# Kernel tuning notes

Hardware: AMD Instinct MI355X
Metric: run time of the kernel (lower is better)

The kernel has to match this reference:

```python
import jax, jax.numpy as jnp
import numpy as np

RADIUS = 0.15
NSAMPLE = 128
NPOINT = 128
EPS = 1e-5  # BatchNorm eps (eval mode, running_mean=0, running_var=1)


def _bn(x, g, b):
    shape = (1, -1) + (1,) * (x.ndim - 2)
    return x * (g / jnp.sqrt(1.0 + EPS)).reshape(shape) + b.reshape(shape)


def _fps(x, npoint):
    # farthest point sampling; x: (Bk, N, 3) -> (Bk, npoint) int32
    Bn, N, _ = x.shape

    def step(carry, _):
        dist, far = carry
        c = jnp.take_along_axis(x, far[:, None, None], 1)  # (Bk,1,3)
        d = jnp.sum((x - c) ** 2, -1)
        dist = jnp.minimum(dist, d)
        return (dist, jnp.argmax(dist, -1).astype(jnp.int32)), far

    init = (jnp.full((Bn, N), 1e10, x.dtype), jnp.zeros((Bn,), jnp.int32))
    _, idxs = jax.lax.scan(step, init, None, length=npoint)
    return idxs.T  # (Bk, npoint)


def _sa_module(x, f, mlp):
    # PointnetSAModuleVotes: FPS -> ball query -> group (use_xyz, normalize_xyz)
    # -> shared MLP (conv2d 1x1 + BN + ReLU) -> max over nsample.
    Bk, M, _ = x.shape
    fps_idx = _fps(x, NPOINT)
    new_xyz = jnp.take_along_axis(x, fps_idx[..., None], 1)  # (Bk,np,3)
    d2 = jnp.sum((new_xyz[:, :, None, :] - x[:, None, :, :]) ** 2, -1)  # (Bk,np,M)
    cand = jnp.where(d2 < RADIUS ** 2, jnp.arange(M)[None, None, :], M)
    cand = jnp.sort(cand, -1)[..., :NSAMPLE]  # first nsample in-radius indices
    first = cand[..., :1]
    first = jnp.where(first == M, 0, first)
    idx = jnp.where(cand == M, first, cand)  # (Bk,np,ns), pad with first valid
    gx = jnp.take_along_axis(x, idx.reshape(Bk, -1)[..., None], 1).reshape(Bk, NPOINT, NSAMPLE, 3)
    gxn = (gx - new_xyz[:, :, None, :]) / RADIUS  # normalize_xyz=True
    gf = jnp.take_along_axis(f[:, :, None, :], idx[:, None, :, :], 3)  # (Bk,C,np,ns)
    h = jnp.concatenate([gxn.transpose(0, 3, 1, 2), gf], 1)  # (Bk, C+3, np, ns)
    for (w, b, g, be) in mlp:
        h = jax.nn.relu(_bn(jnp.einsum('oc,bcps->bops', w, h) + b[None, :, None, None], g, be))
    return new_xyz, h.max(-1)  # (Bk,np,3), (Bk,128,np)


def setup_inputs() -> dict:
    key = jax.random.key(0)
    ks = iter(jax.random.split(key, 40))
    B, M, K, C = 2, 1024, 19, 256
    inp = {}
    inp['xyz'] = jax.random.normal(next(ks), (B, M, K, 3), jnp.float32)
    inp['features'] = jax.random.normal(next(ks), (B, C, K, M), jnp.float32)

    def conv_p(prefix, cin, cout):
        inp[prefix + '_w'] = jax.random.normal(next(ks), (cout, cin), jnp.float32) * (1.0 / np.sqrt(cin))
        inp[prefix + '_b'] = jax.random.normal(next(ks), (cout,), jnp.float32) * 0.02
        inp[prefix + '_g'] = 1.0 + 0.1 * jax.random.normal(next(ks), (cout,), jnp.float32)
        inp[prefix + '_be'] = 0.02 * jax.random.normal(next(ks), (cout,), jnp.float32)

    conv_p('m1', C + 3, 128)  # use_xyz -> 259 in-channels
    conv_p('m2', 128, 128)
    conv_p('m3', 128, 128)
    conv_p('c1', 128, 128)
    conv_p('c2', 128, 128)
    inp['op_w'] = jax.random.normal(next(ks), (K, 5, 128), jnp.float32) * (1.0 / np.sqrt(128))
    inp['op_b'] = jax.random.normal(next(ks), (K, 5), jnp.float32) * 0.02
    return inp


def reference(xyz, features, m1_w, m1_b, m1_g, m1_be, m2_w, m2_b, m2_g, m2_be,
              m3_w, m3_b, m3_g, m3_be, c1_w, c1_b, c1_g, c1_be,
              c2_w, c2_b, c2_g, c2_be, op_w, op_b):
    B, M, K, _ = xyz.shape
    C = features.shape[1]
    # fold vote_factor k into the batch dim (all per-k SA/conv weights are shared)
    x = xyz.transpose(0, 2, 1, 3).reshape(B * K, M, 3)
    f = features.transpose(0, 2, 1, 3).reshape(B * K, C, M)
    mlp = [(m1_w, m1_b, m1_g, m1_be), (m2_w, m2_b, m2_g, m2_be), (m3_w, m3_b, m3_g, m3_be)]
    new_xyz, feat = _sa_module(x, f, mlp)
    net = jax.nn.relu(_bn(jnp.einsum('oc,bcp->bop', c1_w, feat) + c1_b[None, :, None], c1_g, c1_be))
    net = jax.nn.relu(_bn(jnp.einsum('oc,bcp->bop', c2_w, net) + c2_b[None, :, None], c2_g, c2_be))
    net = net.reshape(B, K, 128, NPOINT)
    # per-k output conv (conv_op ModuleList), 128 -> 2+3
    out = jnp.einsum('koc,bkcp->bkop', op_w, net) + op_b[None, :, :, None]
    net_t = out.transpose(0, 1, 3, 2)  # (B,K,np,5)
    agg_xyz = new_xyz.reshape(B, K, NPOINT, 3)
    center = agg_xyz + net_t[..., 2:5]  # decode_scores_
    scores = jnp.concatenate([net_t[..., :2], center], -1)  # obj(2) + center(3)
    return scores, agg_xyz, feat.reshape(B, K, 128, NPOINT)
```

## Files before the change

### kernel.cpp

```cpp
#include <hip/hip_runtime.h>
#include <math.h>

#define NBK   38

#define OFF_XC    0u
#define OFF_NXYZ  466944u
#define OFF_BIDX  525312u
#define OFF_W1F   3015680u
#define OFF_PREP  22938624u
#define OFF_WF    22955008u
#define OFF_CNT   23348224u

#define OUT_AGG   24320
#define OUT_FEAT  38912

typedef short bf16x8 __attribute__((ext_vector_type(8)));
typedef float f32x4  __attribute__((ext_vector_type(4)));
typedef int   v4i    __attribute__((ext_vector_type(4)));
typedef int   v2i    __attribute__((ext_vector_type(2)));

__device__ __forceinline__ float dist2f(float a0, float a1, float a2,
                                        float b0, float b1, float b2) {
#pragma clang fp contract(off)
  float d0 = a0 - b0;
  float d1 = a1 - b1;
  float d2 = a2 - b2;
  return d0 * d0 + d1 * d1 + d2 * d2;
}

__device__ __forceinline__ void split2rn(float v, unsigned& sh, unsigned& sm) {
  unsigned u = __float_as_uint(v);
  unsigned rh = (u + 0x7fffu + ((u >> 16) & 1u)) & 0xffff0000u;
  sh = rh >> 16;
  float r1 = v - __uint_as_float(rh);
  unsigned u1 = __float_as_uint(r1);
  unsigned rm = (u1 + 0x7fffu + ((u1 >> 16) & 1u)) & 0xffff0000u;
  sm = rm >> 16;
}

#define DPP_FMAX_STEP(v, ctrl)                                                 \
  {                                                                            \
    int _s = __builtin_amdgcn_update_dpp(__float_as_int(v), __float_as_int(v), \
                                         (ctrl), 0xf, 0xf, false);             \
    (v) = fmaxf((v), __int_as_float(_s));                                      \
  }

__device__ __forceinline__ float readlane_f(float v, int l) {
  return __int_as_float(__builtin_amdgcn_readlane(__float_as_int(v), l));
}

__global__ __launch_bounds__(512, 2) void front_kernel(
    const float* __restrict__ xyz, const float* __restrict__ feats,
    const float* __restrict__ m1w, const float* __restrict__ m1b,
    const float* __restrict__ m1g, const float* __restrict__ m1be,
    const float* __restrict__ m2w, const float* __restrict__ m2b,
    const float* __restrict__ m2g, const float* __restrict__ m2be,
    const float* __restrict__ m3w, const float* __restrict__ m3b,
    const float* __restrict__ m3g, const float* __restrict__ m3be,
    const float* __restrict__ c1w, const float* __restrict__ c1b,
    const float* __restrict__ c1g, const float* __restrict__ c1be,
    const float* __restrict__ c2w, const float* __restrict__ c2b,
    const float* __restrict__ c2g, const float* __restrict__ c2be,
    float* __restrict__ xc, float* __restrict__ nxyz, float* __restrict__ agg,
    int* __restrict__ bidx, int* __restrict__ counts,
    float* __restrict__ W1f, short* __restrict__ Wf, float* __restrict__ prep)
{
  __shared__ __align__(16) char smem[32768];
  int bid = blockIdx.x, t = threadIdx.x;
  int wave = t >> 6, lane = t & 63;

  if (bid < NBK) {
    int bk = bid;
    int b = bk / 19, k = bk % 19;
    float4* sp4 = (float4*)smem;
    float4* scen4 = (float4*)(smem + 16384);
    int* sfar = (int*)(smem + 18432);
    int2* cexch = (int2*)(smem + 18944);

    for (int i = t; i < 1024; i += 512) {
      const float* src = xyz + ((size_t)((b * 1024 + i) * 19 + k)) * 3;
      float x0 = src[0], x1 = src[1], x2 = src[2];
      sp4[i] = make_float4(x0, x1, x2, 0.f);
      xc[(bk * 3 + 0) * 1024 + i] = x0;
      xc[(bk * 3 + 1) * 1024 + i] = x1;
      xc[(bk * 3 + 2) * 1024 + i] = x2;
    }
    if (t == 0) sfar[0] = 0;
    __syncthreads();

    float px[8], py[8], pz[8], dist[8];
    if (wave < 2) {
      __builtin_amdgcn_s_setprio(1);
      int mbase = (wave << 9) + (lane << 3);
#pragma unroll
      for (int j = 0; j < 8; ++j) {
        float4 p = sp4[mbase + j];
        px[j] = p.x; py[j] = p.y; pz[j] = p.z;
        dist[j] = 1e10f;
      }
    }

    int far = 0;
    for (int it = 1; it < 128; ++it) {
      if (wave < 2) {
        float4 c = sp4[far];
#pragma unroll
        for (int j = 0; j < 8; ++j) {
          float d = dist2f(px[j], py[j], pz[j], c.x, c.y, c.z);
          dist[j] = fminf(dist[j], d);
        }
        float tv[4]; int tj[4];
#pragma unroll
        for (int i = 0; i < 4; ++i) {
          bool L = dist[2 * i] >= dist[2 * i + 1];
          tv[i] = L ? dist[2 * i] : dist[2 * i + 1];
          tj[i] = L ? (2 * i) : (2 * i + 1);
        }
        {
          bool L0 = tv[0] >= tv[1];
          float v0 = L0 ? tv[0] : tv[1]; int j0 = L0 ? tj[0] : tj[1];
          bool L1 = tv[2] >= tv[3];
          float v1 = L1 ? tv[2] : tv[3]; int j1 = L1 ? tj[2] : tj[3];
          bool L = v0 >= v1;
          tv[0] = L ? v0 : v1; tj[0] = L ? j0 : j1;
        }
        float lmax = tv[0];
        float g = lmax;
        DPP_FMAX_STEP(g, 0x111);
        DPP_FMAX_STEP(g, 0x112);
        DPP_FMAX_STEP(g, 0x114);
        DPP_FMAX_STEP(g, 0x118);
        float r0 = readlane_f(g, 15);
        float r1 = readlane_f(g, 31);
        float r2 = readlane_f(g, 47);
        float r3 = readlane_f(g, 63);
        float gmax = fmaxf(fmaxf(r0, r1), fmaxf(r2, r3));
        unsigned long long mk = __ballot(lmax == gmax);
        int wl = (int)__builtin_ctzll(mk);
        int lj = (lane << 3) + tj[0];
        int cand_m = (wave << 9) + __builtin_amdgcn_readlane(lj, wl);
        if (lane == 0) cexch[(it & 1) * 2 + wave] =
            make_int2(__float_as_int(gmax), cand_m);
      }
      __syncthreads();
      if (wave < 2) {
        int2 c0 = cexch[(it & 1) * 2 + 0];
        int2 c1 = cexch[(it & 1) * 2 + 1];
        far = (__int_as_float(c1.x) > __int_as_float(c0.x)) ? c1.y : c0.y;
        if (t == 0) sfar[it] = far;
      }
    }
    if (wave < 2) __builtin_amdgcn_s_setprio(0);
    __syncthreads();

    if (t < 128) {
      float4 c = sp4[sfar[t]];
      scen4[t] = c;
      nxyz[bk * 384 + t * 3 + 0] = c.x;
      nxyz[bk * 384 + t * 3 + 1] = c.y;
      nxyz[bk * 384 + t * 3 + 2] = c.z;
      agg[bk * 384 + t * 3 + 0] = c.x;
      agg[bk * 384 + t * 3 + 1] = c.y;
      agg[bk * 384 + t * 3 + 2] = c.z;
    }
    __syncthreads();

    for (int p = wave * 16; p < wave * 16 + 16; ++p) {
      float4 cen = scen4[p];
      int* outp = bidx + ((size_t)(bk * 128 + p)) * 128;
      int count = 0, first = 0;
      bool got = false;
      for (int ch = 0; ch < 16 && count < 128; ++ch) {
        int m = (ch << 6) + lane;
        float4 pv = sp4[m];
        float d = dist2f(pv.x, pv.y, pv.z, cen.x, cen.y, cen.z);
        bool flag = d < 0.0225f;
        unsigned long long mask = __ballot(flag);
        if (!got && mask) { first = (ch << 6) + __builtin_ctzll(mask); got = true; }
        int pos = count + (int)__popcll(mask & ((1ull << lane) - 1ull));
        if (flag && pos < 128) outp[pos] = m;
        count += (int)__popcll(mask);
      }
      for (int j = count + lane; j < 128; j += 64) outp[j] = first;
      if (lane == 0) counts[bk * 128 + p] = count > 128 ? 128 : count;
    }
    return;
  }

  if (bid < 190) {
    short* ffrag = (short*)smem;
    int blk = bid - NBK;
    int bk = blk >> 2, mq = blk & 3;
    int b = bk / 19, k = bk % 19;
    int quad = lane >> 4, nl = lane & 15;
    int mloc = t & 127, cq = t >> 7;
    int chalf = cq >> 1, ghalf = cq & 1;
    int st_w = mloc >> 4, sl_w = mloc & 15;

    for (int half = 0; half < 2; ++half) {
      int m0 = (mq << 8) + (half << 7);
      const float* fbase = feats + ((size_t)(b * 4864 + k)) * 1024 + m0 + mloc;

      f32x4 acc[8];
#pragma unroll
      for (int st = 0; st < 8; ++st) acc[st] = (f32x4){0.f, 0.f, 0.f, 0.f};

      for (int ch = 0; ch < 4; ++ch) {
        int cbase = ch * 64 + chalf * 32;
#pragma unroll
        for (int g2 = 0; g2 < 2; ++g2) {
          int g = ghalf * 2 + g2;
          float v[8];
#pragma unroll
          for (int j = 0; j < 8; ++j)
            v[j] = fbase[(size_t)(cbase + g * 8 + j) * 19456];
          unsigned sh[8], sm[8];
#pragma unroll
          for (int j = 0; j < 8; ++j) split2rn(v[j], sh[j], sm[j]);
          int base = chalf * 4096 + st_w * 512 + (g * 16 + sl_w) * 8;
          v4i ph = {(int)(sh[0] | (sh[1] << 16)), (int)(sh[2] | (sh[3] << 16)),
                    (int)(sh[4] | (sh[5] << 16)), (int)(sh[6] | (sh[7] << 16))};
          *(v4i*)&ffrag[base] = ph;
          v4i pm = {(int)(sm[0] | (sm[1] << 16)), (int)(sm[2] | (sm[3] << 16)),
                    (int)(sm[4] | (sm[5] << 16)), (int)(sm[6] | (sm[7] << 16))};
          *(v4i*)&ffrag[base + 8192] = pm;
        }
        __syncthreads();
#pragma unroll
        for (int kkl = 0; kkl < 2; ++kkl) {
          int kk = ch * 2 + kkl;
          bf16x8 a0, a1;
          {
            int o_row = wave * 16 + nl;
            const float* wsrc = m1w + o_row * 259 + 3 + kk * 32 + quad * 8;
            float wv[8];
#pragma unroll
            for (int j = 0; j < 8; ++j) wv[j] = wsrc[j];
            unsigned sh[8], sm[8];
#pragma unroll
            for (int j = 0; j < 8; ++j) split2rn(wv[j], sh[j], sm[j]);
            short ah[8], am[8];
#pragma unroll
            for (int j = 0; j < 8; ++j) { ah[j] = (short)sh[j]; am[j] = (short)sm[j]; }
            a0 = (bf16x8){ah[0], ah[1], ah[2], ah[3], ah[4], ah[5], ah[6], ah[7]};
            a1 = (bf16x8){am[0], am[1], am[2], am[3], am[4], am[5], am[6], am[7]};
          }
#pragma unroll
          for (int st = 0; st < 8; ++st) {
            const short* hb = ffrag + kkl * 4096 + st * 512 + lane * 8;
            bf16x8 b0 = *(const bf16x8*)hb;
            bf16x8 b1 = *(const bf16x8*)(hb + 8192);
            f32x4 c = acc[st];
            c = __builtin_amdgcn_mfma_f32_16x16x32_bf16(a1, b0, c, 0, 0, 0);
            c = __builtin_amdgcn_mfma_f32_16x16x32_bf16(a0, b1, c, 0, 0, 0);
            c = __builtin_amdgcn_mfma_f32_16x16x32_bf16(a0, b0, c, 0, 0, 0);
            acc[st] = c;
          }
        }
        __syncthreads();
      }
      float inv = 1.0f / sqrtf(1.0f + 1e-5f);
      int o0 = wave * 16 + quad * 4;
      float4 bb = *(const float4*)&m1b[o0];
      float4 gg = *(const float4*)&m1g[o0];
#pragma unroll
      for (int st = 0; st < 8; ++st) {
        int m_out = m0 + st * 16 + nl;
        f32x4 cc = acc[st];
        float4 r;
        r.x = (cc[0] + bb.x) * (gg.x * inv);
        r.y = (cc[1] + bb.y) * (gg.y * inv);
        r.z = (cc[2] + bb.z) * (gg.z * inv);
        r.w = (cc[3] + bb.w) * (gg.w * inv);
        *(float4*)&W1f[((size_t)(bk * 1024 + m_out)) * 128 + o0] = r;
      }
    }
    return;
  }

  if (bid < 206) {
    int idx = (bid - 190) * 512 + t;
#pragma unroll
    for (int e = 0; e < 4; ++e) {
      int i = idx * 4 + e;
      int c = i & 127, o = (i >> 7) & 127, l = i >> 14;
      float w = (l ? m3w : m2w)[o * 128 + c];
      unsigned sh, sm;
      split2rn(w, sh, sm);
      int ot = o >> 4, mm = o & 15, kk = c >> 5, q = (c & 31) >> 3, j = c & 7;
      int within = (q * 16 + mm) * 8 + j;
      Wf[(((l * 2 + 0) * 4 + kk) * 8 + ot) * 512 + within] = (short)sh;
      Wf[(((l * 2 + 1) * 4 + kk) * 8 + ot) * 512 + within] = (short)sm;
    }
    return;
  }

  if (bid < 222) {
    int idx2 = (bid - 206) * 512 + t;
#pragma unroll
    for (int e = 0; e < 4; ++e) {
      int i = idx2 * 4 + e;
      int c = i & 127, o = (i >> 7) & 127, l = i >> 14;
      float w = (l ? c2w : c1w)[o * 128 + c];
      unsigned sh, sm;
      split2rn(w, sh, sm);
      int ot = o >> 4, mm = o & 15, kk = c >> 5, q = (c & 31) >> 3, j = c & 7;
      int within = (q * 16 + mm) * 8 + j;
      Wf[131072 + (((l * 2 + 0) * 4 + kk) * 8 + ot) * 512 + within] = (short)sh;
      Wf[131072 + (((l * 2 + 1) * 4 + kk) * 8 + ot) * 512 + within] = (short)sm;
    }
    return;
  }

  if (t < 128) {
    float inv = 1.0f / sqrtf(1.0f + 1e-5f);
    float a1 = m1g[t] * inv;
    prep[t] = a1;
    float a2 = m2g[t] * inv;  prep[256 + t] = a2;  prep[384 + t] = fmaf(m2b[t], a2, m2be[t]);
    float a3 = m3g[t] * inv;  prep[512 + t] = a3;  prep[640 + t] = fmaf(m3b[t], a3, m3be[t]);
    float ac1 = c1g[t] * inv; prep[768 + t] = ac1; prep[896 + t] = fmaf(c1b[t], ac1, c1be[t]);
    float ac2 = c2g[t] * inv; prep[1024 + t] = ac2; prep[1152 + t] = fmaf(c2b[t], ac2, c2be[t]);
    prep[1280 + 4 * t + 0] = m1w[t * 259 + 0] * a1;
    prep[1280 + 4 * t + 1] = m1w[t * 259 + 1] * a1;
    prep[1280 + 4 * t + 2] = m1w[t * 259 + 2] * a1;
    prep[1280 + 4 * t + 3] = m1be[t];
  }
}

__device__ __forceinline__ void mfma_layer(const short* __restrict__ Wf,
                                           const short* hfrag, int l,
                                           int wave, int lane, int nst_h,
                                           f32x4 acc[2][4])
{
#pragma unroll 1
  for (int kk = 0; kk < 4; ++kk) {
    bf16x8 a[2][2];
#pragma unroll
    for (int oi = 0; oi < 2; ++oi)
#pragma unroll
      for (int sp = 0; sp < 2; ++sp)
        a[oi][sp] = *(const bf16x8*)(Wf + (((l * 2 + sp) * 4 + kk) * 8 + (wave * 2 + oi)) * 512 + lane * 8);
    for (int st = 0; st < nst_h; ++st) {
      const short* hb = hfrag + kk * 2048 + st * 512 + lane * 8;
      bf16x8 b0 = *(const bf16x8*)(hb);
      bf16x8 b1 = *(const bf16x8*)(hb + 8192);
#pragma unroll
      for (int oi = 0; oi < 2; ++oi) {
        f32x4 c = acc[oi][st];
        c = __builtin_amdgcn_mfma_f32_16x16x32_bf16(a[oi][1], b0, c, 0, 0, 0);
        c = __builtin_amdgcn_mfma_f32_16x16x32_bf16(a[oi][0], b1, c, 0, 0, 0);
        c = __builtin_amdgcn_mfma_f32_16x16x32_bf16(a[oi][0], b0, c, 0, 0, 0);
        acc[oi][st] = c;
      }
    }
  }
}

__global__ __launch_bounds__(256, 3) void sa_kernel(
    const float* __restrict__ xc, const float* __restrict__ nxyz,
    const int* __restrict__ bidx, const int* __restrict__ counts,
    const float* __restrict__ W1f, const float* __restrict__ prep,
    const short* __restrict__ Wf, float* __restrict__ feat_out)
{
  __shared__ __align__(16) short hfrag[16384];
  __shared__ float pcs[512];
  __shared__ float sm[32 * 128];
  __shared__ float ccen[12];
  __shared__ int scnt[4];
  int gb = blockIdx.x, bk = gb >> 5, pb = (gb & 31) << 2;
  int t = threadIdx.x;
  int wave = t >> 6, lane = t & 63;
  int quad = lane >> 4, nl = lane & 15;

  pcs[t] = prep[1280 + t];
  pcs[256 + t] = prep[1536 + t];
  if (t < 4) scnt[t] = counts[bk * 128 + pb + t];
  if (t < 12) {
    int bb = t / 3, c = t % 3;
    ccen[t] = nxyz[(bk * 128 + pb + bb) * 3 + c];
  }
  __syncthreads();
  int n0 = (scnt[0] + 15) >> 4, n1 = (scnt[1] + 15) >> 4;
  int n2 = (scnt[2] + 15) >> 4, n3 = (scnt[3] + 15) >> 4;
  int pf1 = n0, pf2 = n0 + n1, pf3 = n0 + n1 + n2, T = n0 + n1 + n2 + n3;

  for (int q0 = 0; q0 < T; q0 += 4) {
    int nst_h = T - q0;
    if (nst_h > 4) nst_h = 4;
    {
      int cg = wave;
      int st = lane >> 4, sl = lane & 15;
      if (st < nst_h) {
        int q = q0 + st;
        int bq = (q >= pf1) + (q >= pf2) + (q >= pf3);
        int tstart = (bq == 0) ? 0 : (bq == 1) ? pf1 : (bq == 2) ? pf2 : pf3;
        int tslot = q - tstart;
        int m = bidx[((size_t)(bk * 128 + pb + bq)) * 128 + tslot * 16 + sl];
        float cen0 = ccen[bq * 3 + 0], cen1 = ccen[bq * 3 + 1], cen2 = ccen[bq * 3 + 2];
        float g0 = (xc[(bk * 3 + 0) * 1024 + m] - cen0) * (1.0f / 0.15f);
        float g1 = (xc[(bk * 3 + 1) * 1024 + m] - cen1) * (1.0f / 0.15f);
        float g2 = (xc[(bk * 3 + 2) * 1024 + m] - cen2) * (1.0f / 0.15f);
        const float4* wrow = (const float4*)(W1f + ((size_t)(bk * 1024 + m)) * 128 + cg * 32);
        const float4* pcp = (const float4*)pcs + cg * 32;
#pragma unroll
        for (int g = 0; g < 4; ++g) {
          float4 wva = wrow[g * 2], wvb = wrow[g * 2 + 1];
          float wv[8] = {wva.x, wva.y, wva.z, wva.w, wvb.x, wvb.y, wvb.z, wvb.w};
          unsigned sh[8], smv[8];
#pragma unroll
          for (int e = 0; e < 8; ++e) {
            float4 pc = pcp[g * 8 + e];
            float hv = fmaxf(wv[e] + pc.x * g0 + pc.y * g1 + pc.z * g2 + pc.w, 0.f);
            split2rn(hv, sh[e], smv[e]);
          }
          int base = (cg * 4 + st) * 512 + (g * 16 + sl) * 8;
          v4i ph = {(int)(sh[0] | (sh[1] << 16)), (int)(sh[2] | (sh[3] << 16)),
                    (int)(sh[4] | (sh[5] << 16)), (int)(sh[6] | (sh[7] << 16))};
          *(v4i*)&hfrag[base] = ph;
          v4i pm = {(int)(smv[0] | (smv[1] << 16)), (int)(smv[2] | (smv[3] << 16)),
                    (int)(smv[4] | (smv[5] << 16)), (int)(smv[6] | (smv[7] << 16))};
          *(v4i*)&hfrag[base + 8192] = pm;
        }
      }
    }
    __syncthreads();

    f32x4 acc[2][4];
#pragma unroll
    for (int oi = 0; oi < 2; ++oi)
#pragma unroll
      for (int st = 0; st < 4; ++st) acc[oi][st] = (f32x4){0.f, 0.f, 0.f, 0.f};
    mfma_layer(Wf, hfrag, 0, wave, lane, nst_h, acc);
    __syncthreads();

#pragma unroll
    for (int oi = 0; oi < 2; ++oi) {
      int o0 = (wave * 2 + oi) * 16 + quad * 4;
      float4 al = *(const float4*)&prep[256 + o0];
      float4 be = *(const float4*)&prep[384 + o0];
      int kk2 = o0 >> 5, g2 = (o0 & 31) >> 3, j0 = o0 & 7;
      for (int st = 0; st < nst_h; ++st) {
        f32x4 cc = acc[oi][st];
        float v0 = fmaxf(fmaf(cc[0], al.x, be.x), 0.f);
        float v1 = fmaxf(fmaf(cc[1], al.y, be.y), 0.f);
        float v2 = fmaxf(fmaf(cc[2], al.z, be.z), 0.f);
        float v3 = fmaxf(fmaf(cc[3], al.w, be.w), 0.f);
        unsigned h0, m0_, h1, m1_, h2, m2_, h3, m3_;
        split2rn(v0, h0, m0_); split2rn(v1, h1, m1_);
        split2rn(v2, h2, m2_); split2rn(v3, h3, m3_);
        int base = (kk2 * 4 + st) * 512 + (g2 * 16 + nl) * 8 + j0;
        v2i w0 = {(int)(h0 | (h1 << 16)), (int)(h2 | (h3 << 16))};
        *(v2i*)&hfrag[base] = w0;
        v2i w1 = {(int)(m0_ | (m1_ << 16)), (int)(m2_ | (m3_ << 16))};
        *(v2i*)&hfrag[base + 8192] = w1;
      }
    }
    __syncthreads();

#pragma unroll
    for (int oi = 0; oi < 2; ++oi)
#pragma unroll
      for (int st = 0; st < 4; ++st) acc[oi][st] = (f32x4){0.f, 0.f, 0.f, 0.f};
    mfma_layer(Wf, hfrag, 1, wave, lane, nst_h, acc);

#pragma unroll
    for (int oi = 0; oi < 2; ++oi) {
      int o0 = (wave * 2 + oi) * 16 + quad * 4;
      float4 al = *(const float4*)&prep[512 + o0];
      float4 be = *(const float4*)&prep[640 + o0];
      for (int st = 0; st < nst_h; ++st) {
        f32x4 cc = acc[oi][st];
        float v[4];
        v[0] = fmaxf(fmaf(cc[0], al.x, be.x), 0.f);
        v[1] = fmaxf(fmaf(cc[1], al.y, be.y), 0.f);
        v[2] = fmaxf(fmaf(cc[2], al.z, be.z), 0.f);
        v[3] = fmaxf(fmaf(cc[3], al.w, be.w), 0.f);
#pragma unroll
        for (int r = 0; r < 4; ++r) {
          float x = v[r];
          x = fmaxf(x, __shfl_xor(x, 1));
          x = fmaxf(x, __shfl_xor(x, 2));
          x = fmaxf(x, __shfl_xor(x, 4));
          x = fmaxf(x, __shfl_xor(x, 8));
          if (nl == 0) sm[(q0 + st) * 128 + o0 + r] = x;
        }
      }
    }
    __syncthreads();
  }

#pragma unroll
  for (int e = t; e < 512; e += 256) {
    int bb = e >> 7, o = e & 127;
    int qs = (bb == 0) ? 0 : (bb == 1) ? pf1 : (bb == 2) ? pf2 : pf3;
    int nq = (bb == 0) ? n0 : (bb == 1) ? n1 : (bb == 2) ? n2 : n3;
    float v = sm[qs * 128 + o];
    for (int q = 1; q < nq; ++q) v = fmaxf(v, sm[(qs + q) * 128 + o]);
    feat_out[(((size_t)bk) << 14) + (o << 7) + pb + bb] = v;
  }
}

__global__ __launch_bounds__(256) void head_kernel(const float* __restrict__ featg,
    const float* __restrict__ prep, const short* __restrict__ Wf,
    const float* __restrict__ nxyz, const float* __restrict__ opw,
    const float* __restrict__ opb, float* __restrict__ scores)
{
  __shared__ __align__(16) short hfrag[16384];
  __shared__ float hplain[128 * 65];
  int bk = blockIdx.x >> 1, p0 = (blockIdx.x & 1) << 6;
  int t = threadIdx.x;
  int wave = t >> 6, lane = t & 63;
  int quad = lane >> 4, nl = lane & 15;
  const short* WC = Wf + 131072;

  {
    int cg = wave;
    int st = lane >> 4, sl = lane & 15;
    const float* fb = featg + (bk << 14) + p0 + lane;
#pragma unroll
    for (int g = 0; g < 4; ++g) {
      float v[8];
#pragma unroll
      for (int e = 0; e < 8; ++e)
        v[e] = fb[(cg * 32 + g * 8 + e) << 7];
      unsigned sh[8], sm[8];
#pragma unroll
      for (int e = 0; e < 8; ++e) split2rn(v[e], sh[e], sm[e]);
      int base = (cg * 4 + st) * 512 + (g * 16 + sl) * 8;
      v4i ph = {(int)(sh[0] | (sh[1] << 16)), (int)(sh[2] | (sh[3] << 16)),
                (int)(sh[4] | (sh[5] << 16)), (int)(sh[6] | (sh[7] << 16))};
      *(v4i*)&hfrag[base] = ph;
      v4i pm = {(int)(sm[0] | (sm[1] << 16)), (int)(sm[2] | (sm[3] << 16)),
                (int)(sm[4] | (sm[5] << 16)), (int)(sm[6] | (sm[7] << 16))};
      *(v4i*)&hfrag[base + 8192] = pm;
    }
  }
  __syncthreads();

  f32x4 acc[2][4];
#pragma unroll
  for (int oi = 0; oi < 2; ++oi)
#pragma unroll
    for (int st = 0; st < 4; ++st) acc[oi][st] = (f32x4){0.f, 0.f, 0.f, 0.f};
  mfma_layer(WC, hfrag, 0, wave, lane, 4, acc);
  __syncthreads();

#pragma unroll
  for (int oi = 0; oi < 2; ++oi) {
    int o0 = (wave * 2 + oi) * 16 + quad * 4;
    float4 al = *(const float4*)&prep[768 + o0];
    float4 be = *(const float4*)&prep[896 + o0];
    int kk2 = o0 >> 5, g2 = (o0 & 31) >> 3, j0 = o0 & 7;
#pragma unroll
    for (int st = 0; st < 4; ++st) {
      f32x4 cc = acc[oi][st];
      float v0 = fmaxf(fmaf(cc[0], al.x, be.x), 0.f);
      float v1 = fmaxf(fmaf(cc[1], al.y, be.y), 0.f);
      float v2 = fmaxf(fmaf(cc[2], al.z, be.z), 0.f);
      float v3 = fmaxf(fmaf(cc[3], al.w, be.w), 0.f);
      unsigned h0, m0_, h1, m1_, h2, m2_, h3, m3_;
      split2rn(v0, h0, m0_); split2rn(v1, h1, m1_);
      split2rn(v2, h2, m2_); split2rn(v3, h3, m3_);
      int base = (kk2 * 4 + st) * 512 + (g2 * 16 + nl) * 8 + j0;
      v2i w0 = {(int)(h0 | (h1 << 16)), (int)(h2 | (h3 << 16))};
      *(v2i*)&hfrag[base] = w0;
      v2i w1 = {(int)(m0_ | (m1_ << 16)), (int)(m2_ | (m3_ << 16))};
      *(v2i*)&hfrag[base + 8192] = w1;
    }
  }
  __syncthreads();

#pragma unroll
  for (int oi = 0; oi < 2; ++oi)
#pragma unroll
    for (int st = 0; st < 4; ++st) acc[oi][st] = (f32x4){0.f, 0.f, 0.f, 0.f};
  mfma_layer(WC, hfrag, 1, wave, lane, 4, acc);

#pragma unroll
  for (int oi = 0; oi < 2; ++oi) {
    int o0 = (wave * 2 + oi) * 16 + quad * 4;
    float4 al = *(const float4*)&prep[1024 + o0];
    float4 be = *(const float4*)&prep[1152 + o0];
#pragma unroll
    for (int st = 0; st < 4; ++st) {
      f32x4 cc = acc[oi][st];
      int p = st * 16 + nl;
      hplain[(o0 + 0) * 65 + p] = fmaxf(fmaf(cc[0], al.x, be.x), 0.f);
      hplain[(o0 + 1) * 65 + p] = fmaxf(fmaf(cc[1], al.y, be.y), 0.f);
      hplain[(o0 + 2) * 65 + p] = fmaxf(fmaf(cc[2], al.z, be.z), 0.f);
      hplain[(o0 + 3) * 65 + p] = fmaxf(fmaf(cc[3], al.w, be.w), 0.f);
    }
  }
  __syncthreads();

  if (t < 64) {
    int p = t, k = bk % 19;
    float res[5];
#pragma unroll
    for (int j = 0; j < 5; ++j) {
      const float* wr = opw + ((size_t)(k * 5 + j)) * 128;
      float a = opb[k * 5 + j];
      for (int c = 0; c < 128; ++c) a = fmaf(wr[c], hplain[c * 65 + p], a);
      res[j] = a;
    }
    int pg = p0 + p;
    float a0 = nxyz[(bk * 128 + pg) * 3 + 0];
    float a1 = nxyz[(bk * 128 + pg) * 3 + 1];
    float a2 = nxyz[(bk * 128 + pg) * 3 + 2];
    float* sc = scores + ((size_t)(bk * 128 + pg)) * 5;
    sc[0] = res[0];
    sc[1] = res[1];
    sc[2] = a0 + res[2];
    sc[3] = a1 + res[3];
    sc[4] = a2 + res[4];
  }
}

extern "C" void kernel_launch(void* const* d_in, const int* in_sizes, int n_in,
                              void* d_out, int out_size, void* d_ws, size_t ws_size,
                              hipStream_t stream) {
  (void)in_sizes; (void)n_in; (void)out_size; (void)ws_size;
  const float* xyz  = (const float*)d_in[0];
  const float* fts  = (const float*)d_in[1];
  const float* m1w  = (const float*)d_in[2];
  const float* m1b  = (const float*)d_in[3];
  const float* m1g  = (const float*)d_in[4];
  const float* m1be = (const float*)d_in[5];
  const float* m2w  = (const float*)d_in[6];
  const float* m2b  = (const float*)d_in[7];
  const float* m2g  = (const float*)d_in[8];
  const float* m2be = (const float*)d_in[9];
  const float* m3w  = (const float*)d_in[10];
  const float* m3b  = (const float*)d_in[11];
  const float* m3g  = (const float*)d_in[12];
  const float* m3be = (const float*)d_in[13];
  const float* c1w  = (const float*)d_in[14];
  const float* c1b  = (const float*)d_in[15];
  const float* c1g  = (const float*)d_in[16];
  const float* c1be = (const float*)d_in[17];
  const float* c2w  = (const float*)d_in[18];
  const float* c2b  = (const float*)d_in[19];
  const float* c2g  = (const float*)d_in[20];
  const float* c2be = (const float*)d_in[21];
  const float* opw  = (const float*)d_in[22];
  const float* opb  = (const float*)d_in[23];

  float* out = (float*)d_out;
  char* ws = (char*)d_ws;
  float* xc   = (float*)(ws + OFF_XC);
  float* nxyz = (float*)(ws + OFF_NXYZ);
  int*   bidx = (int*)(ws + OFF_BIDX);
  float* W1f  = (float*)(ws + OFF_W1F);
  float* prep = (float*)(ws + OFF_PREP);
  short* Wf   = (short*)(ws + OFF_WF);
  int*   cnt  = (int*)(ws + OFF_CNT);

  hipLaunchKernelGGL(front_kernel, dim3(223), dim3(512), 0, stream,
                     xyz, fts, m1w, m1b, m1g, m1be, m2w, m2b, m2g, m2be,
                     m3w, m3b, m3g, m3be, c1w, c1b, c1g, c1be,
                     c2w, c2b, c2g, c2be,
                     xc, nxyz, out + OUT_AGG, bidx, cnt, W1f, Wf, prep);
  hipLaunchKernelGGL(sa_kernel, dim3(NBK * 32), dim3(256), 0, stream,
                     xc, nxyz, bidx, cnt, W1f, prep, Wf, out + OUT_FEAT);
  hipLaunchKernelGGL(head_kernel, dim3(NBK * 2), dim3(256), 0, stream,
                     out + OUT_FEAT, prep, Wf, nxyz, opw, opb, out);
}
```

Measured before the change: 283.8 us.

## Spread FPS across all eight waves with two points per lane

Farthest point sampling now uses all 8 waves of the block, each lane holding 2 points instead of 8, in place of only 2 waves each holding 8 points per lane. Each wave publishes its max and index to shared memory, and every thread reduces the 8 candidates after the barrier. This shortens the per-lane serial distance and argmax work on the latency-bound FPS loop, in exchange for a barrier across 8 waves and 8 LDS reads per iteration. The wave priority boost is removed. Tie-breaking still picks the lowest index, since the cross-wave reduction uses a strict greater-than.

```diff
diff --git a/kernel.cpp b/kernel.cpp
--- a/kernel.cpp
+++ b/kernel.cpp
@@ -88,69 +88,55 @@
     if (t == 0) sfar[0] = 0;
     __syncthreads();
 
-    float px[8], py[8], pz[8], dist[8];
-    if (wave < 2) {
-      __builtin_amdgcn_s_setprio(1);
-      int mbase = (wave << 9) + (lane << 3);
-#pragma unroll
-      for (int j = 0; j < 8; ++j) {
-        float4 p = sp4[mbase + j];
-        px[j] = p.x; py[j] = p.y; pz[j] = p.z;
-        dist[j] = 1e10f;
-      }
+    float px[2], py[2], pz[2], dist[2];
+    int mbase = (wave << 7) + (lane << 1);
+#pragma unroll
+    for (int j = 0; j < 2; ++j) {
+      float4 p = sp4[mbase + j];
+      px[j] = p.x; py[j] = p.y; pz[j] = p.z;
+      dist[j] = 1e10f;
     }
 
     int far = 0;
     for (int it = 1; it < 128; ++it) {
-      if (wave < 2) {
-        float4 c = sp4[far];
-#pragma unroll
-        for (int j = 0; j < 8; ++j) {
-          float d = dist2f(px[j], py[j], pz[j], c.x, c.y, c.z);
-          dist[j] = fminf(dist[j], d);
-        }
-        float tv[4]; int tj[4];
-#pragma unroll
-        for (int i = 0; i < 4; ++i) {
-          bool L = dist[2 * i] >= dist[2 * i + 1];
-          tv[i] = L ? dist[2 * i] : dist[2 * i + 1];
-          tj[i] = L ? (2 * i) : (2 * i + 1);
-        }
-        {
-          bool L0 = tv[0] >= tv[1];
-          float v0 = L0 ? tv[0] : tv[1]; int j0 = L0 ? tj[0] : tj[1];
-          bool L1 = tv[2] >= tv[3];
-          float v1 = L1 ? tv[2] : tv[3]; int j1 = L1 ? tj[2] : tj[3];
-          bool L = v0 >= v1;
-          tv[0] = L ? v0 : v1; tj[0] = L ? j0 : j1;
-        }
-        float lmax = tv[0];
-        float g = lmax;
-        DPP_FMAX_STEP(g, 0x111);
-        DPP_FMAX_STEP(g, 0x112);
-        DPP_FMAX_STEP(g, 0x114);
-        DPP_FMAX_STEP(g, 0x118);
-        float r0 = readlane_f(g, 15);
-        float r1 = readlane_f(g, 31);
-        float r2 = readlane_f(g, 47);
-        float r3 = readlane_f(g, 63);
-        float gmax = fmaxf(fmaxf(r0, r1), fmaxf(r2, r3));
-        unsigned long long mk = __ballot(lmax == gmax);
-        int wl = (int)__builtin_ctzll(mk);
-        int lj = (lane << 3) + tj[0];
-        int cand_m = (wave << 9) + __builtin_amdgcn_readlane(lj, wl);
-        if (lane == 0) cexch[(it & 1) * 2 + wave] =
-            make_int2(__float_as_int(gmax), cand_m);
-      }
+      float4 c = sp4[far];
+      float d0 = dist2f(px[0], py[0], pz[0], c.x, c.y, c.z);
+      float d1 = dist2f(px[1], py[1], pz[1], c.x, c.y, c.z);
+      dist[0] = fminf(dist[0], d0);
+      dist[1] = fminf(dist[1], d1);
+      bool L = dist[0] >= dist[1];
+      float lmax = L ? dist[0] : dist[1];
+      int lj = (lane << 1) + (L ? 0 : 1);
+      float g = lmax;
+      DPP_FMAX_STEP(g, 0x111);
+      DPP_FMAX_STEP(g, 0x112);
+      DPP_FMAX_STEP(g, 0x114);
+      DPP_FMAX_STEP(g, 0x118);
+      float r0 = readlane_f(g, 15);
+      float r1 = readlane_f(g, 31);
+      float r2 = readlane_f(g, 47);
+      float r3 = readlane_f(g, 63);
+      float gmax = fmaxf(fmaxf(r0, r1), fmaxf(r2, r3));
+      unsigned long long mk = __ballot(lmax == gmax);
+      int wl = (int)__builtin_ctzll(mk);
+      int cand_m = (wave << 7) + __builtin_amdgcn_readlane(lj, wl);
+      if (lane == 0) cexch[(it & 1) * 8 + wave] =
+          make_int2(__float_as_int(gmax), cand_m);
       __syncthreads();
-      if (wave < 2) {
-        int2 c0 = cexch[(it & 1) * 2 + 0];
-        int2 c1 = cexch[(it & 1) * 2 + 1];
-        far = (__int_as_float(c1.x) > __int_as_float(c0.x)) ? c1.y : c0.y;
-        if (t == 0) sfar[it] = far;
-      }
-    }
-    if (wave < 2) __builtin_amdgcn_s_setprio(0);
+      int2 cc = cexch[(it & 1) * 8 + 0];
+      float bd = __int_as_float(cc.x);
+      int bm = cc.y;
+#pragma unroll
+      for (int w = 1; w < 8; ++w) {
+        int2 cw = cexch[(it & 1) * 8 + w];
+        float dw = __int_as_float(cw.x);
+        bool G = dw > bd;
+        bd = G ? dw : bd;
+        bm = G ? cw.y : bm;
+      }
+      far = bm;
+      if (t == 0) sfar[it] = far;
+    }
     __syncthreads();
 
     if (t < 128) {
```

New measurement: 282.5 us. No clear change (-0.5%).

## Run FPS in a single wave with padded LDS point layout

Applied to the files above, without the earlier changes.

Farthest point sampling now runs in one wavefront holding 16 points per lane instead of two wavefronts. That removes the per-iteration __syncthreads and the shared-memory exchange of candidates between the waves. Points are re-read from LDS every iteration instead of being kept in registers, and the LDS layout is padded by one float4 per 16 entries to avoid bank conflicts on the strided per-lane reads. The cost is twice the serial distance work per lane and extra LDS traffic on the critical FPS loop.

```diff
diff --git a/kernel.cpp b/kernel.cpp
--- a/kernel.cpp
+++ b/kernel.cpp
@@ -72,15 +72,14 @@
   if (bid < NBK) {
     int bk = bid;
     int b = bk / 19, k = bk % 19;
-    float4* sp4 = (float4*)smem;
-    float4* scen4 = (float4*)(smem + 16384);
-    int* sfar = (int*)(smem + 18432);
-    int2* cexch = (int2*)(smem + 18944);
+    float4* sp4p = (float4*)smem;
+    float4* scen4 = (float4*)(smem + 17408);
+    int* sfar = (int*)(smem + 19456);
 
     for (int i = t; i < 1024; i += 512) {
       const float* src = xyz + ((size_t)((b * 1024 + i) * 19 + k)) * 3;
       float x0 = src[0], x1 = src[1], x2 = src[2];
-      sp4[i] = make_float4(x0, x1, x2, 0.f);
+      sp4p[i + (i >> 4)] = make_float4(x0, x1, x2, 0.f);
       xc[(bk * 3 + 0) * 1024 + i] = x0;
       xc[(bk * 3 + 1) * 1024 + i] = x1;
       xc[(bk * 3 + 2) * 1024 + i] = x2;
@@ -88,41 +87,36 @@
     if (t == 0) sfar[0] = 0;
     __syncthreads();
 
-    float px[8], py[8], pz[8], dist[8];
-    if (wave < 2) {
-      __builtin_amdgcn_s_setprio(1);
-      int mbase = (wave << 9) + (lane << 3);
-#pragma unroll
-      for (int j = 0; j < 8; ++j) {
-        float4 p = sp4[mbase + j];
-        px[j] = p.x; py[j] = p.y; pz[j] = p.z;
-        dist[j] = 1e10f;
-      }
-    }
-
-    int far = 0;
-    for (int it = 1; it < 128; ++it) {
-      if (wave < 2) {
-        float4 c = sp4[far];
-#pragma unroll
-        for (int j = 0; j < 8; ++j) {
-          float d = dist2f(px[j], py[j], pz[j], c.x, c.y, c.z);
+    if (wave == 0) {
+      float dist[16];
+#pragma unroll
+      for (int j = 0; j < 16; ++j) dist[j] = 1e10f;
+      int far = 0;
+      for (int it = 1; it < 128; ++it) {
+        float4 c = sp4p[far + (far >> 4)];
+        int bq = lane * 17;
+        asm volatile("" : "+v"(bq));
+#pragma unroll
+        for (int j = 0; j < 16; ++j) {
+          float4 p = sp4p[bq + j];
+          float d = dist2f(p.x, p.y, p.z, c.x, c.y, c.z);
           dist[j] = fminf(dist[j], d);
         }
-        float tv[4]; int tj[4];
-#pragma unroll
-        for (int i = 0; i < 4; ++i) {
+        float tv[8]; int tj[8];
+#pragma unroll
+        for (int i = 0; i < 8; ++i) {
           bool L = dist[2 * i] >= dist[2 * i + 1];
           tv[i] = L ? dist[2 * i] : dist[2 * i + 1];
           tj[i] = L ? (2 * i) : (2 * i + 1);
         }
-        {
-          bool L0 = tv[0] >= tv[1];
-          float v0 = L0 ? tv[0] : tv[1]; int j0 = L0 ? tj[0] : tj[1];
-          bool L1 = tv[2] >= tv[3];
-          float v1 = L1 ? tv[2] : tv[3]; int j1 = L1 ? tj[2] : tj[3];
-          bool L = v0 >= v1;
-          tv[0] = L ? v0 : v1; tj[0] = L ? j0 : j1;
+#pragma unroll
+        for (int s = 1; s < 8; s <<= 1) {
+#pragma unroll
+          for (int i = 0; i < 8; i += 2 * s) {
+            bool L = tv[i] >= tv[i + s];
+            tv[i] = L ? tv[i] : tv[i + s];
+            tj[i] = L ? tj[i] : tj[i + s];
+          }
         }
         float lmax = tv[0];
         float g = lmax;
@@ -137,24 +131,15 @@
         float gmax = fmaxf(fmaxf(r0, r1), fmaxf(r2, r3));
         unsigned long long mk = __ballot(lmax == gmax);
         int wl = (int)__builtin_ctzll(mk);
-        int lj = (lane << 3) + tj[0];
-        int cand_m = (wave << 9) + __builtin_amdgcn_readlane(lj, wl);
-        if (lane == 0) cexch[(it & 1) * 2 + wave] =
-            make_int2(__float_as_int(gmax), cand_m);
-      }
-      __syncthreads();
-      if (wave < 2) {
-        int2 c0 = cexch[(it & 1) * 2 + 0];
-        int2 c1 = cexch[(it & 1) * 2 + 1];
-        far = (__int_as_float(c1.x) > __int_as_float(c0.x)) ? c1.y : c0.y;
-        if (t == 0) sfar[it] = far;
-      }
-    }
-    if (wave < 2) __builtin_amdgcn_s_setprio(0);
+        far = __builtin_amdgcn_readlane((lane << 4) + tj[0], wl);
+        if (lane == 0) sfar[it] = far;
+      }
+    }
     __syncthreads();
 
     if (t < 128) {
-      float4 c = sp4[sfar[t]];
+      int fm = sfar[t];
+      float4 c = sp4p[fm + (fm >> 4)];
       scen4[t] = c;
       nxyz[bk * 384 + t * 3 + 0] = c.x;
       nxyz[bk * 384 + t * 3 + 1] = c.y;
@@ -172,7 +157,7 @@
       bool got = false;
       for (int ch = 0; ch < 16 && count < 128; ++ch) {
         int m = (ch << 6) + lane;
-        float4 pv = sp4[m];
+        float4 pv = sp4p[m + (m >> 4)];
         float d = dist2f(pv.x, pv.y, pv.z, cen.x, cen.y, cen.z);
         bool flag = d < 0.0225f;
         unsigned long long mask = __ballot(flag);
```

Result: slower. 323.5 us (+14.0%).

## Split farthest point sampling into a separate 128-thread kernel before front kernel

Applied to the files above, without the earlier changes.

Moves the FPS loop out of the 512-thread front_kernel blocks into its own kernel with 128-thread blocks, so the per-iteration barrier involves only the two working waves instead of eight mostly idle ones. The front kernel now reloads the point coordinates and sampled centers from global memory for the ball query. This adds a kernel launch and serializes FPS ahead of the other front_kernel work (weight prep etc.), which previously ran concurrently in the other blocks.

```diff
diff --git a/kernel.cpp b/kernel.cpp
--- a/kernel.cpp
+++ b/kernel.cpp
@@ -47,6 +47,95 @@
 
 __device__ __forceinline__ float readlane_f(float v, int l) {
   return __int_as_float(__builtin_amdgcn_readlane(__float_as_int(v), l));
+}
+
+__global__ __launch_bounds__(128, 1) void fps_kernel(
+    const float* __restrict__ xyz, float* __restrict__ xc,
+    float* __restrict__ nxyz, float* __restrict__ agg)
+{
+  __shared__ __align__(16) float4 sp4[1024];
+  __shared__ int2 cexch[2][2];
+  __shared__ int sfar[128];
+  int bk = blockIdx.x;
+  int b = bk / 19, k = bk % 19;
+  int t = threadIdx.x, lane = t & 63, wave = t >> 6;
+
+  for (int i = t; i < 1024; i += 128) {
+    const float* src = xyz + ((size_t)((b * 1024 + i) * 19 + k)) * 3;
+    float x0 = src[0], x1 = src[1], x2 = src[2];
+    sp4[i] = make_float4(x0, x1, x2, 0.f);
+    xc[(bk * 3 + 0) * 1024 + i] = x0;
+    xc[(bk * 3 + 1) * 1024 + i] = x1;
+    xc[(bk * 3 + 2) * 1024 + i] = x2;
+  }
+  if (t == 0) sfar[0] = 0;
+  __syncthreads();
+
+  float px[8], py[8], pz[8], dist[8];
+  int mbase = (wave << 9) + (lane << 3);
+#pragma unroll
+  for (int j = 0; j < 8; ++j) {
+    float4 p = sp4[mbase + j];
+    px[j] = p.x; py[j] = p.y; pz[j] = p.z;
+    dist[j] = 1e10f;
+  }
+
+  int far = 0;
+  for (int it = 1; it < 128; ++it) {
+    float4 c = sp4[far];
+#pragma unroll
+    for (int j = 0; j < 8; ++j) {
+      float d = dist2f(px[j], py[j], pz[j], c.x, c.y, c.z);
+      dist[j] = fminf(dist[j], d);
+    }
+    float tv[4]; int tj[4];
+#pragma unroll
+    for (int i = 0; i < 4; ++i) {
+      bool L = dist[2 * i] >= dist[2 * i + 1];
+      tv[i] = L ? dist[2 * i] : dist[2 * i + 1];
+      tj[i] = L ? (2 * i) : (2 * i + 1);
+    }
+    {
+      bool L0 = tv[0] >= tv[1];
+      float v0 = L0 ? tv[0] : tv[1]; int j0 = L0 ? tj[0] : tj[1];
+      bool L1 = tv[2] >= tv[3];
+      float v1 = L1 ? tv[2] : tv[3]; int j1 = L1 ? tj[2] : tj[3];
+      bool L = v0 >= v1;
+      tv[0] = L ? v0 : v1; tj[0] = L ? j0 : j1;
+    }
+    float lmax = tv[0];
+    float g = lmax;
+    DPP_FMAX_STEP(g, 0x111);
+    DPP_FMAX_STEP(g, 0x112);
+    DPP_FMAX_STEP(g, 0x114);
+    DPP_FMAX_STEP(g, 0x118);
+    float r0 = readlane_f(g, 15);
+    float r1 = readlane_f(g, 31);
+    float r2 = readlane_f(g, 47);
+    float r3 = readlane_f(g, 63);
+    float gmax = fmaxf(fmaxf(r0, r1), fmaxf(r2, r3));
+    unsigned long long mk = __ballot(lmax == gmax);
+    int wl = (int)__builtin_ctzll(mk);
+    int lj = (lane << 3) + tj[0];
+    int cand_m = (wave << 9) + __builtin_amdgcn_readlane(lj, wl);
+    if (lane == 0) cexch[it & 1][wave] = make_int2(__float_as_int(gmax), cand_m);
+    __syncthreads();
+    int2 c0 = cexch[it & 1][0];
+    int2 c1 = cexch[it & 1][1];
+    far = (__int_as_float(c1.x) > __int_as_float(c0.x)) ? c1.y : c0.y;
+    if (t == 0) sfar[it] = far;
+  }
+  __syncthreads();
+
+  if (t < 128) {
+    float4 c = sp4[sfar[t]];
+    nxyz[bk * 384 + t * 3 + 0] = c.x;
+    nxyz[bk * 384 + t * 3 + 1] = c.y;
+    nxyz[bk * 384 + t * 3 + 2] = c.z;
+    agg[bk * 384 + t * 3 + 0] = c.x;
+    agg[bk * 384 + t * 3 + 1] = c.y;
+    agg[bk * 384 + t * 3 + 2] = c.z;
+  }
 }
 
 __global__ __launch_bounds__(512, 2) void front_kernel(
@@ -61,7 +150,7 @@
     const float* __restrict__ c1g, const float* __restrict__ c1be,
     const float* __restrict__ c2w, const float* __restrict__ c2b,
     const float* __restrict__ c2g, const float* __restrict__ c2be,
-    float* __restrict__ xc, float* __restrict__ nxyz, float* __restrict__ agg,
+    float* __restrict__ xc, float* __restrict__ nxyz,
     int* __restrict__ bidx, int* __restrict__ counts,
     float* __restrict__ W1f, short* __restrict__ Wf, float* __restrict__ prep)
 {
@@ -71,97 +160,20 @@
 
   if (bid < NBK) {
     int bk = bid;
-    int b = bk / 19, k = bk % 19;
-    float4* sp4 = (float4*)smem;
-    float4* scen4 = (float4*)(smem + 16384);
-    int* sfar = (int*)(smem + 18432);
-    int2* cexch = (int2*)(smem + 18944);
+    float* sx0 = (float*)smem;
+    float* sx1 = sx0 + 1024;
+    float* sx2 = sx1 + 1024;
+    float4* scen4 = (float4*)(smem + 12288);
 
     for (int i = t; i < 1024; i += 512) {
-      const float* src = xyz + ((size_t)((b * 1024 + i) * 19 + k)) * 3;
-      float x0 = src[0], x1 = src[1], x2 = src[2];
-      sp4[i] = make_float4(x0, x1, x2, 0.f);
-      xc[(bk * 3 + 0) * 1024 + i] = x0;
-      xc[(bk * 3 + 1) * 1024 + i] = x1;
-      xc[(bk * 3 + 2) * 1024 + i] = x2;
-    }
-    if (t == 0) sfar[0] = 0;
-    __syncthreads();
-
-    float px[8], py[8], pz[8], dist[8];
-    if (wave < 2) {
-      __builtin_amdgcn_s_setprio(1);
-      int mbase = (wave << 9) + (lane << 3);
-#pragma unroll
-      for (int j = 0; j < 8; ++j) {
-        float4 p = sp4[mbase + j];
-        px[j] = p.x; py[j] = p.y; pz[j] = p.z;
-        dist[j] = 1e10f;
-      }
-    }
-
-    int far = 0;
-    for (int it = 1; it < 128; ++it) {
-      if (wave < 2) {
-        float4 c = sp4[far];
-#pragma unroll
-        for (int j = 0; j < 8; ++j) {
-          float d = dist2f(px[j], py[j], pz[j], c.x, c.y, c.z);
-          dist[j] = fminf(dist[j], d);
-        }
-        float tv[4]; int tj[4];
-#pragma unroll
-        for (int i = 0; i < 4; ++i) {
-          bool L = dist[2 * i] >= dist[2 * i + 1];
-          tv[i] = L ? dist[2 * i] : dist[2 * i + 1];
-          tj[i] = L ? (2 * i) : (2 * i + 1);
-        }
-        {
-          bool L0 = tv[0] >= tv[1];
-          float v0 = L0 ? tv[0] : tv[1]; int j0 = L0 ? tj[0] : tj[1];
-          bool L1 = tv[2] >= tv[3];
-          float v1 = L1 ? tv[2] : tv[3]; int j1 = L1 ? tj[2] : tj[3];
-          bool L = v0 >= v1;
-          tv[0] = L ? v0 : v1; tj[0] = L ? j0 : j1;
-        }
-        float lmax = tv[0];
-        float g = lmax;
-        DPP_FMAX_STEP(g, 0x111);
-        DPP_FMAX_STEP(g, 0x112);
-        DPP_FMAX_STEP(g, 0x114);
-        DPP_FMAX_STEP(g, 0x118);
-        float r0 = readlane_f(g, 15);
-        float r1 = readlane_f(g, 31);
-        float r2 = readlane_f(g, 47);
-        float r3 = readlane_f(g, 63);
-        float gmax = fmaxf(fmaxf(r0, r1), fmaxf(r2, r3));
-        unsigned long long mk = __ballot(lmax == gmax);
-        int wl = (int)__builtin_ctzll(mk);
-        int lj = (lane << 3) + tj[0];
-        int cand_m = (wave << 9) + __builtin_amdgcn_readlane(lj, wl);
-        if (lane == 0) cexch[(it & 1) * 2 + wave] =
-            make_int2(__float_as_int(gmax), cand_m);
-      }
-      __syncthreads();
-      if (wave < 2) {
-        int2 c0 = cexch[(it & 1) * 2 + 0];
-        int2 c1 = cexch[(it & 1) * 2 + 1];
-        far = (__int_as_float(c1.x) > __int_as_float(c0.x)) ? c1.y : c0.y;
-        if (t == 0) sfar[it] = far;
-      }
-    }
-    if (wave < 2) __builtin_amdgcn_s_setprio(0);
-    __syncthreads();
-
+      sx0[i] = xc[(bk * 3 + 0) * 1024 + i];
+      sx1[i] = xc[(bk * 3 + 1) * 1024 + i];
+      sx2[i] = xc[(bk * 3 + 2) * 1024 + i];
+    }
     if (t < 128) {
-      float4 c = sp4[sfar[t]];
-      scen4[t] = c;
-      nxyz[bk * 384 + t * 3 + 0] = c.x;
-      nxyz[bk * 384 + t * 3 + 1] = c.y;
-      nxyz[bk * 384 + t * 3 + 2] = c.z;
-      agg[bk * 384 + t * 3 + 0] = c.x;
-      agg[bk * 384 + t * 3 + 1] = c.y;
-      agg[bk * 384 + t * 3 + 2] = c.z;
+      scen4[t] = make_float4(nxyz[(bk * 128 + t) * 3 + 0],
+                             nxyz[(bk * 128 + t) * 3 + 1],
+                             nxyz[(bk * 128 + t) * 3 + 2], 0.f);
     }
     __syncthreads();
 
@@ -172,8 +184,7 @@
       bool got = false;
       for (int ch = 0; ch < 16 && count < 128; ++ch) {
         int m = (ch << 6) + lane;
-        float4 pv = sp4[m];
-        float d = dist2f(pv.x, pv.y, pv.z, cen.x, cen.y, cen.z);
+        float d = dist2f(sx0[m], sx1[m], sx2[m], cen.x, cen.y, cen.z);
         bool flag = d < 0.0225f;
         unsigned long long mask = __ballot(flag);
         if (!got && mask) { first = (ch << 6) + __builtin_ctzll(mask); got = true; }
@@ -655,11 +666,13 @@
   short* Wf   = (short*)(ws + OFF_WF);
   int*   cnt  = (int*)(ws + OFF_CNT);
 
+  hipLaunchKernelGGL(fps_kernel, dim3(NBK), dim3(128), 0, stream,
+                     xyz, xc, nxyz, out + OUT_AGG);
   hipLaunchKernelGGL(front_kernel, dim3(223), dim3(512), 0, stream,
                      xyz, fts, m1w, m1b, m1g, m1be, m2w, m2b, m2g, m2be,
                      m3w, m3b, m3g, m3be, c1w, c1b, c1g, c1be,
                      c2w, c2b, c2g, c2be,
-                     xc, nxyz, out + OUT_AGG, bidx, cnt, W1f, Wf, prep);
+                     xc, nxyz, bidx, cnt, W1f, Wf, prep);
   hipLaunchKernelGGL(sa_kernel, dim3(NBK * 32), dim3(256), 0, stream,
                      xc, nxyz, bidx, cnt, W1f, prep, Wf, out + OUT_FEAT);
   hipLaunchKernelGGL(head_kernel, dim3(NBK * 2), dim3(256), 0, stream,
```

Result: no change. 288.0 us (+1.5%).
